# Optimization experiments

Hardware: AMD Instinct MI355X
Metric: run time of the kernel (lower is better)

Reference implementation:

```python
import jax, jax.numpy as jnp
import numpy as np

EPS = 1e-5
DIL = 1
PAD = 1
STRIDE = 1

def conv2d(x, w, stride=1, pad=1, dil=1):
    return jax.lax.conv_general_dilated(x, w, (stride, stride), [(pad, pad), (pad, pad)],
                                        rhs_dilation=(dil, dil),
                                        dimension_numbers=('NCHW', 'OIHW', 'NCHW'))

def batchnorm(x, g, b, m, v):
    inv = g / jnp.sqrt(v + EPS)
    return x * inv[None, :, None, None] + (b - m * inv)[None, :, None, None]

def _bilinear(img, y, x):
    # img: [C,H,W]; y,x: [Ho,Wo] float sample coords; zero padding outside.
    H, W = img.shape[1], img.shape[2]
    y0 = jnp.floor(y); x0 = jnp.floor(x)
    ty = y - y0; tx = x - x0
    y0i = y0.astype(jnp.int32); x0i = x0.astype(jnp.int32)
    def g(yi, xi):
        valid = (yi >= 0) & (yi < H) & (xi >= 0) & (xi < W)
        v = img[:, jnp.clip(yi, 0, H - 1), jnp.clip(xi, 0, W - 1)]  # [C,Ho,Wo]
        return jnp.where(valid[None], v, jnp.zeros((), img.dtype))
    return (g(y0i, x0i) * ((1 - ty) * (1 - tx))[None]
            + g(y0i, x0i + 1) * ((1 - ty) * tx)[None]
            + g(y0i + 1, x0i) * (ty * (1 - tx))[None]
            + g(y0i + 1, x0i + 1) * (ty * tx)[None])

def deform_conv(x, w, offset, stride=1, pad=1, dil=1):
    # offset: [B, 18, Ho, Wo], channels 0:9 = dy per kernel tap (row-major), 9:18 = dx.
    B, C, H, W = x.shape
    Co = w.shape[0]
    Ho = (H + 2 * pad - dil * 2 - 1) // stride + 1
    Wo = (W + 2 * pad - dil * 2 - 1) // stride + 1
    off = offset.reshape(B, 2, 9, Ho, Wo)
    iy = (jnp.arange(Ho) * stride - pad).astype(x.dtype)
    ix = (jnp.arange(Wo) * stride - pad).astype(x.dtype)
    wk = w.reshape(Co, C, 9)
    out = jnp.zeros((B, Co, Ho, Wo), x.dtype)
    for k in range(9):  # fixed 3x3 kernel taps
        ky, kx = k // 3, k % 3
        ys = iy[:, None] + ky * dil + off[:, 0, k]  # [B,Ho,Wo]
        xs = ix[None, :] + kx * dil + off[:, 1, k]
        val = jax.vmap(_bilinear)(x, ys, xs)        # [B,C,Ho,Wo]
        out = out + jnp.einsum('bchw,oc->bohw', val, wk[:, :, k])
    return out

def offset_bias(dil, dtype):
    bw = jnp.array([[-1., 0., 1.]] * 3, dtype) * (dil - 1)
    bh = bw.T
    return jnp.concatenate([bh.reshape(-1), bw.reshape(-1)])  # [18]

def setup_inputs() -> dict:
    key = jax.random.key(0)
    ks = jax.random.split(key, 12)
    B, C, H, W = 8, 256, 56, 56
    inp = {
        'x': jax.random.normal(ks[0], (B, C, H, W), jnp.float32),
        'conv1_w': jax.random.normal(ks[1], (C, C, 3, 3), jnp.float32) * 0.02,
        'bn1_g': jax.random.normal(ks[2], (C,), jnp.float32) * 0.1 + 1.0,
        'bn1_b': jax.random.normal(ks[3], (C,), jnp.float32) * 0.1,
        'bn1_m': jax.random.normal(ks[4], (C,), jnp.float32) * 0.1,
        'bn1_v': jax.random.uniform(ks[5], (C,), jnp.float32) + 0.5,
        'off_w': jax.random.normal(ks[6], (18, C, 3, 3), jnp.float32) * 0.01,
        'off_b': jnp.zeros((18,), jnp.float32),
        'conv2_w': jax.random.normal(ks[7], (C, C, 3, 3), jnp.float32) * 0.02,
        'bn2_g': jax.random.normal(ks[8], (C,), jnp.float32) * 0.1 + 1.0,
        'bn2_b': jax.random.normal(ks[9], (C,), jnp.float32) * 0.1,
        'bn2_m': jax.random.normal(ks[10], (C,), jnp.float32) * 0.1,
        'bn2_v': jax.random.uniform(ks[11], (C,), jnp.float32) + 0.5,
    }
    return inp

def reference(x, conv1_w, bn1_g, bn1_b, bn1_m, bn1_v, off_w, off_b, conv2_w, bn2_g, bn2_b, bn2_m, bn2_v):
    residual = x
    out = conv2d(x, conv1_w, STRIDE, PAD, DIL)
    out = jax.nn.relu(batchnorm(out, bn1_g, bn1_b, bn1_m, bn1_v))
    offset = conv2d(out, off_w, STRIDE, PAD, DIL) + off_b[None, :, None, None]
    offset = offset + offset_bias(DIL, out.dtype)[None, :, None, None]
    out = deform_conv(out, conv2_w, offset, STRIDE, PAD, DIL)
    out = batchnorm(out, bn2_g, bn2_b, bn2_m, bn2_v)
    return jax.nn.relu(out + residual)
```

## Files before the change

kernel.cpp:

```cpp
#include <hip/hip_runtime.h>
#include <hip/hip_fp16.h>

#define NB 8
#define NH 56
#define NW 56
#define NHW 3136
#define NCHW 802816
#define NPIX 25088
#define NHP 58
#define EPSV 1e-5f
#define BUFS 20480
#define TOFN 451584

typedef float f32x4 __attribute__((ext_vector_type(4)));
typedef __bf16 bf16x8 __attribute__((ext_vector_type(8)));
typedef _Float16 f16x8 __attribute__((ext_vector_type(8)));

__device__ __forceinline__ unsigned short f2b(float f) {
  unsigned int u = __float_as_uint(f);
  u += 0x7FFFu + ((u >> 16) & 1u);
  return (unsigned short)(u >> 16);
}
__device__ __forceinline__ unsigned short f2h(float f) {
  return __half_as_ushort(__float2half(f));
}
__device__ __forceinline__ void soft_barrier() {
  __builtin_amdgcn_s_waitcnt(0xC07F);
  __builtin_amdgcn_s_barrier();
}
__device__ __forceinline__ void dma16(const unsigned short* g, unsigned short* l) {
  __builtin_amdgcn_global_load_lds(
      (const __attribute__((address_space(1))) unsigned int*)g,
      (__attribute__((address_space(3))) unsigned int*)l,
      16, 0, 0);
}
__device__ __forceinline__ unsigned int bil2(
    unsigned int c00, unsigned int c01, unsigned int c10, unsigned int c11,
    __half2 W00, __half2 W01, __half2 W10, __half2 W11) {
  __half2 v = __hmul2(W00, *(__half2*)&c00);
  v = __hfma2(W01, *(__half2*)&c01, v);
  v = __hfma2(W10, *(__half2*)&c10, v);
  v = __hfma2(W11, *(__half2*)&c11, v);
  return *(unsigned int*)&v;
}

__global__ __launch_bounds__(256) void prep_fused(
    const float* __restrict__ x,  unsigned short* __restrict__ xbp,
    unsigned short* __restrict__ t1b, float* __restrict__ tof,
    const float* __restrict__ w1, const float* __restrict__ w2,
    const float* __restrict__ ow,
    unsigned short* __restrict__ w1p, unsigned short* __restrict__ w2p,
    unsigned short* __restrict__ w3p)
{
  __shared__ float T[64][65];
  const int bid = blockIdx.x;
  const int tid = threadIdx.x;

  if (bid < 228) {
    int i = bid*256 + tid;
    int q = i & 31; int pid = i >> 5;
    int b = pid / 228, j = pid % 228;
    int y, xx;
    if (j < 58)       { y = 0;  xx = j; }
    else if (j < 116) { y = 57; xx = j - 58; }
    else { int jj = j - 116; y = 1 + (jj >> 1); xx = (jj & 1) * 57; }
    size_t addr = ((size_t)(b*NHP + y)*NHP + xx)*256 + q*8;
    uint4 z = make_uint4(0u,0u,0u,0u);
    *(uint4*)(xbp + addr) = z;
    *(uint4*)(t1b + addr) = z;
    int zi = i*8;
    if (zi < TOFN) {
      *(float4*)(tof + zi)     = make_float4(0.f,0.f,0.f,0.f);
      *(float4*)(tof + zi + 4) = make_float4(0.f,0.f,0.f,0.f);
    }
  } else if (bid < 1796) {
    const int j2   = bid - 228;
    const int pxt  = (j2 % 392) * 64;
    const int cg   = (j2 / 392) * 64;
    const int b    = pxt / NHW;
    const int rem0 = pxt % NHW;
    const int pl   = tid & 63;
    const int c0   = tid >> 6;
    const float* src = x + (size_t)b*NCHW + rem0;
    #pragma unroll
    for (int it = 0; it < 16; ++it) {
      int c = c0 + it*4;
      T[c][pl] = src[(size_t)(cg + c)*NHW + pl];
    }
    __syncthreads();
    const int pr = tid >> 5;
    const int cp = tid & 31;
    #pragma unroll
    for (int it = 0; it < 8; ++it) {
      int pxl = pr + it*8;
      int rem = rem0 + pxl;
      int ho = rem / NW, wo = rem % NW;
      unsigned int pk = ((unsigned int)f2b(T[cp*2+1][pxl]) << 16) | (unsigned int)f2b(T[cp*2][pxl]);
      *(unsigned int*)(xbp + ((size_t)(b*NHP + ho + 1)*NHP + (wo + 1))*256 + cg + cp*2) = pk;
    }
  } else {
    int i = (bid - 1796)*256 + tid;
    if (i < 589824) {
      int co = i / 2304, r = i % 2304, k = r >> 8, ci = r & 255;
      w1p[i] = f2b(w1[((size_t)co*256 + ci)*9 + k]);
    } else if (i < 1179648) {
      int j = i - 589824;
      int co = j / 2304, r = j % 2304, k = r >> 8, ci = r & 255;
      w2p[j] = f2h(w2[((size_t)co*256 + ci)*9 + k]);
    } else {
      int j = i - 1179648;
      int co = j / 2304, r = j % 2304, k = r >> 8, ci = r & 255;
      w3p[j] = (co < 18) ? f2h(ow[((size_t)co*256 + ci)*9 + k]) : (unsigned short)0;
    }
  }
}

__global__ __launch_bounds__(512, 4) void gemm_conv1(
    const unsigned short* __restrict__ xbp, const unsigned short* __restrict__ w1p,
    const float* __restrict__ gam, const float* __restrict__ bet,
    const float* __restrict__ mu,  const float* __restrict__ var,
    unsigned short* __restrict__ t1b)
{
  __shared__ unsigned short SMEM[2*BUFS];

  const int bx   = blockIdx.x;
  const int nbx  = (bx & 7)*49 + (bx >> 3);
  const int m0   = nbx * 64;
  const int t    = threadIdx.x;
  const int lane = t & 63;
  const int wv   = t >> 6;
  const int wvM  = wv & 1;
  const int wvN  = wv >> 1;
  const int quad = lane >> 4;
  const int l15  = lane & 15;

  const int srow = t >> 3;
  const int seg  = t & 7;
  const int swz8 = ((seg ^ (srow & 7))*8);
  const int px  = m0 + srow;
  const int b   = px / NHW, rem = px % NHW;
  const int ho  = rem / NW, wo = rem % NW;
  const unsigned int pbaseA = ((unsigned int)(b*NHP + ho)*NHP + wo)*256u + (unsigned int)swz8;
  const int rowB0 = wv*32 + (lane >> 3);
  const unsigned int bswz = (unsigned int)(((lane & 7) ^ (lane >> 3))*8);
  const int chA = wv*512;

  f32x4 acc[2][4];
  #pragma unroll
  for (int i = 0; i < 2; ++i)
    #pragma unroll
    for (int j = 0; j < 4; ++j) acc[i][j] = (f32x4)(0.f);

  {
    dma16(xbp + pbaseA, &SMEM[chA]);
    #pragma unroll
    for (int j = 0; j < 4; ++j)
      dma16(w1p + (size_t)(rowB0 + j*8)*2304 + bswz, &SMEM[4096 + (wv*4 + j)*512]);
    __syncthreads();
  }

  for (int r = 0; r < 36; ++r) {
    unsigned short* Ac = SMEM + (r & 1)*BUFS;
    unsigned short* Bc = Ac + 4096;
    unsigned short* An = SMEM + ((r + 1) & 1)*BUFS;
    unsigned short* Bn = An + 4096;
    if (r < 35) {
      const int rn = r + 1;
      const int kn = rn >> 2, cicn = rn & 3;
      const int kyn = kn/3, kxn = kn - kyn*3;
      const unsigned int koff = (unsigned int)((kyn*NHP + kxn)*256 + cicn*64);
      dma16(xbp + pbaseA + koff, &An[chA]);
      const unsigned int rb = (unsigned int)(rn*64);
      #pragma unroll
      for (int j = 0; j < 4; ++j)
        dma16(w1p + (size_t)(rowB0 + j*8)*2304 + rb + bswz, &Bn[(wv*4 + j)*512]);
    }
    #pragma unroll
    for (int kk = 0; kk < 2; ++kk) {
      const int s8 = (kk*4 + quad) ^ (l15 & 7);
      bf16x8 af[2], bfr[4];
      #pragma unroll
      for (int mt = 0; mt < 2; ++mt)
        af[mt] = *(const bf16x8*)(&Ac[(wvM*32 + mt*16 + l15)*64 + s8*8]);
      #pragma unroll
      for (int nt = 0; nt < 4; ++nt)
        bfr[nt] = *(const bf16x8*)(&Bc[(wvN*64 + nt*16 + l15)*64 + s8*8]);
      #pragma unroll
      for (int mt = 0; mt < 2; ++mt)
        #pragma unroll
        for (int nt = 0; nt < 4; ++nt)
          acc[mt][nt] = __builtin_amdgcn_mfma_f32_16x16x32_bf16(af[mt], bfr[nt], acc[mt][nt], 0, 0, 0);
    }
    __syncthreads();
  }

  unsigned short* Sw = SMEM + wv*2304;
  #pragma unroll
  for (int nt = 0; nt < 4; ++nt) {
    const int co = wvN*64 + nt*16 + l15;
    const float inv  = gam[co] * rsqrtf(var[co] + EPSV);
    const float beta = bet[co] - mu[co]*inv;
    #pragma unroll
    for (int mt = 0; mt < 2; ++mt) {
      #pragma unroll
      for (int rr = 0; rr < 4; ++rr) {
        const int pxl = mt*16 + quad*4 + rr;
        float val = acc[mt][nt][rr]*inv + beta;
        val = val > 0.f ? val : 0.f;
        Sw[pxl*72 + nt*16 + l15] = f2h(val);
      }
    }
  }
  #pragma unroll
  for (int i = 0; i < 4; ++i) {
    const int pxl = (lane >> 3) + 8*i;
    const int sc  = lane & 7;
    uint4 q = *(const uint4*)(&Sw[pxl*72 + sc*8]);
    const int pg = m0 + wvM*32 + pxl;
    const int bb = pg / NHW, rm = pg % NHW;
    const int hh = rm / NW, ww = rm % NW;
    *(uint4*)(t1b + ((size_t)(bb*NHP + hh + 1)*NHP + ww + 1)*256 + wvN*64 + sc*8) = q;
  }
}

__global__ __launch_bounds__(256, 8) void gemm_off(
    const unsigned short* __restrict__ t1b, const unsigned short* __restrict__ w3p,
    const float* __restrict__ ob, float* __restrict__ toff)
{
  __shared__ unsigned short Al[4096];
  __shared__ unsigned short Bl[2048];

  const int bx  = blockIdx.x;
  const int nbx = (bx & 7)*49 + (bx >> 3);
  const int m0  = nbx * 64;
  const int kc = blockIdx.y;
  const int t    = threadIdx.x;
  const int lane = t & 63;
  const int wv   = t >> 6;
  const int quad = lane >> 4;
  const int l15  = lane & 15;

  const int arow = t >> 2;
  const int as4  = t & 3;
  const int axor = arow & 7;
  const int pxa  = m0 + arow;
  const int ba   = pxa / NHW, rema = pxa % NHW;
  const unsigned int pbase = ((unsigned int)(ba*NHP + rema/NW)*NHP + rema%NW)*256u;

  const int brow = t >> 3;
  const int bs   = t & 7;

  f32x4 acc[2];
  #pragma unroll
  for (int nt = 0; nt < 2; ++nt) {
    float init = 0.f;
    if (kc == 0) { int co = nt*16 + l15; init = (co < 18) ? ob[co] : 0.f; }
    acc[nt] = (f32x4)(init);
  }

  uint4 pA0, pA1, pB;
  {
    const int r = kc*9, k = r >> 2, cic = r & 3;
    const int ky = k/3, kx = k - ky*3;
    const unsigned int base = pbase + (unsigned int)((ky*NHP + kx)*256 + cic*64);
    pA0 = *(const uint4*)(t1b + base + as4*8);
    pA1 = *(const uint4*)(t1b + base + (as4+4)*8);
    pB  = *(const uint4*)(w3p + (size_t)brow*2304 + r*64 + bs*8);
  }

  for (int rr = 0; rr < 9; ++rr) {
    const int r = kc*9 + rr;
    __syncthreads();
    *(uint4*)(&Al[arow*64 + ((as4     ^ axor)*8)]) = pA0;
    *(uint4*)(&Al[arow*64 + (((as4+4) ^ axor)*8)]) = pA1;
    *(uint4*)(&Bl[brow*64 + ((bs ^ (brow & 7))*8)]) = pB;
    {
      const int rn = (rr < 8) ? r + 1 : r;
      const int kn = rn >> 2, cicn = rn & 3;
      const int kyn = kn/3, kxn = kn - kyn*3;
      const unsigned int base = pbase + (unsigned int)((kyn*NHP + kxn)*256 + cicn*64);
      pA0 = *(const uint4*)(t1b + base + as4*8);
      pA1 = *(const uint4*)(t1b + base + (as4+4)*8);
      pB  = *(const uint4*)(w3p + (size_t)brow*2304 + rn*64 + bs*8);
    }
    soft_barrier();
    #pragma unroll
    for (int kk = 0; kk < 2; ++kk) {
      const int s8 = (kk*4 + quad) ^ (l15 & 7);
      f16x8 af = *(const f16x8*)(&Al[(wv*16 + l15)*64 + s8*8]);
      #pragma unroll
      for (int nt = 0; nt < 2; ++nt) {
        f16x8 bfr = *(const f16x8*)(&Bl[(nt*16 + l15)*64 + s8*8]);
        acc[nt] = __builtin_amdgcn_mfma_f32_16x16x32_f16(af, bfr, acc[nt], 0, 0, 0);
      }
    }
  }
  #pragma unroll
  for (int nt = 0; nt < 2; ++nt) {
    const int co = nt*16 + l15;
    if (co < 18) {
      #pragma unroll
      for (int rr2 = 0; rr2 < 4; ++rr2) {
        const int pg = m0 + wv*16 + quad*4 + rr2;
        const int bb = pg / NHW, rm = pg % NHW;
        atomicAdd(&toff[(size_t)bb*(18*NHW) + (size_t)co*NHW + rm], acc[nt][rr2]);
      }
    }
  }
}

__global__ __launch_bounds__(512, 4) void gemm_deform(
    const unsigned short* __restrict__ t1b, const unsigned short* __restrict__ w2p,
    const float* __restrict__ toff, const float* __restrict__ xres,
    const float* __restrict__ gam, const float* __restrict__ bet,
    const float* __restrict__ mu,  const float* __restrict__ var,
    float* __restrict__ outp)
{
  __shared__ unsigned short SMEM[2*BUFS];

  const int bid  = blockIdx.x;
  const int nb   = (bid & 7)*49 + (bid >> 3);
  const int m0   = nb * 64;
  const int t    = threadIdx.x;
  const int lane = t & 63;
  const int wv   = t >> 6;
  const int wvM  = wv & 1;
  const int wvN  = wv >> 1;
  const int quad = lane >> 4;
  const int l15  = lane & 15;

  const int srow = t >> 3;
  const int seg  = t & 7;
  const int sxor = srow & 7;
  const int px   = m0 + srow;
  const int b    = px / NHW, rem = px % NHW;
  const int ho   = rem / NW, wo = rem % NW;
  const int obb  = b*(18*NHW) + rem;
  const unsigned int prowb = (unsigned int)(b*NHP);

  const int rowB0 = wv*32 + (lane >> 3);
  const unsigned int bswz = (unsigned int)(((lane & 7) ^ (lane >> 3))*8);

  f32x4 acc[2][4];
  #pragma unroll
  for (int i = 0; i < 2; ++i)
    #pragma unroll
    for (int j = 0; j < 4; ++j) acc[i][j] = (f32x4)(0.f);

  unsigned int o00, o01, o10, o11;
  __half2 W00, W01, W10, W11;
#define COORDS(KK) {                                                   \
    const int ky_ = (KK)/3, kx_ = (KK) - ky_*3;                        \
    const float offy = toff[obb + (KK)*NHW];                           \
    const float offx = toff[obb + (9+(KK))*NHW];                       \
    const float yf = (float)(ho - 1 + ky_) + offy;                     \
    const float xf = (float)(wo - 1 + kx_) + offx;                     \
    const float y0f = floorf(yf), x0f = floorf(xf);                    \
    const float ty = yf - y0f,   tx = xf - x0f;                        \
    const int y0p = (int)y0f + 1, x0p = (int)x0f + 1;                  \
    const int cy0 = min(max(y0p,   0), NHP-1);                         \
    const int cy1 = min(max(y0p+1, 0), NHP-1);                         \
    const int cx0 = min(max(x0p,   0), NHP-1);                         \
    const int cx1 = min(max(x0p+1, 0), NHP-1);                         \
    W00 = __float2half2_rn((1.f-ty)*(1.f-tx));                         \
    W01 = __float2half2_rn((1.f-ty)*tx);                               \
    W10 = __float2half2_rn(ty*(1.f-tx));                               \
    W11 = __float2half2_rn(ty*tx);                                     \
    o00 = ((prowb + cy0)*NHP + cx0)*256u + seg*8u;                     \
    o01 = ((prowb + cy0)*NHP + cx1)*256u + seg*8u;                     \
    o10 = ((prowb + cy1)*NHP + cx0)*256u + seg*8u;                     \
    o11 = ((prowb + cy1)*NHP + cx1)*256u + seg*8u;                     \
  }

#define PACKW(DST) {                                                            \
    uint4 res;                                                                  \
    res.x = bil2(pc00.x, pc01.x, pc10.x, pc11.x, W00, W01, W10, W11);           \
    res.y = bil2(pc00.y, pc01.y, pc10.y, pc11.y, W00, W01, W10, W11);           \
    res.z = bil2(pc00.z, pc01.z, pc10.z, pc11.z, W00, W01, W10, W11);           \
    res.w = bil2(pc00.w, pc01.w, pc10.w, pc11.w, W00, W01, W10, W11);           \
    *(uint4*)(&(DST)[srow*64 + ((seg ^ sxor)*8)]) = res;                        \
  }

#define ISSUEC(RN) {                                                           \
    const unsigned int cio_ = (unsigned int)(((RN) & 3)*64);                   \
    pc00 = *(const uint4*)(t1b + o00 + cio_);                                  \
    pc01 = *(const uint4*)(t1b + o01 + cio_);                                  \
    pc10 = *(const uint4*)(t1b + o10 + cio_);                                  \
    pc11 = *(const uint4*)(t1b + o11 + cio_);                                  \
  }

  uint4 pc00, pc01, pc10, pc11;

  COORDS(0);
  {
    ISSUEC(0);
    #pragma unroll
    for (int j = 0; j < 4; ++j)
      dma16(w2p + (size_t)(rowB0 + j*8)*2304 + bswz, &SMEM[4096 + (wv*4 + j)*512]);
    PACKW(SMEM);
    ISSUEC(1);
    __syncthreads();
  }

  for (int r = 0; r < 36; ++r) {
    unsigned short* Ac = SMEM + (r & 1)*BUFS;
    unsigned short* Bc = Ac + 4096;
    unsigned short* An = SMEM + ((r + 1) & 1)*BUFS;
    unsigned short* Bn = An + 4096;
    if (r < 35) PACKW(An);
    if (r < 35) {
      const unsigned int rb = (unsigned int)((r + 1)*64);
      #pragma unroll
      for (int j = 0; j < 4; ++j)
        dma16(w2p + (size_t)(rowB0 + j*8)*2304 + rb + bswz, &Bn[(wv*4 + j)*512]);
    }
    if ((r & 3) == 2 && r < 34) COORDS((r + 2) >> 2);
    if (r < 34) {
      ISSUEC(r + 2);
    }
    #pragma unroll
    for (int kk = 0; kk < 2; ++kk) {
      const int s8 = (kk*4 + quad) ^ (l15 & 7);
      f16x8 af[2], bfr[4];
      #pragma unroll
      for (int mt = 0; mt < 2; ++mt)
        af[mt] = *(const f16x8*)(&Ac[(wvM*32 + mt*16 + l15)*64 + s8*8]);
      #pragma unroll
      for (int nt = 0; nt < 4; ++nt)
        bfr[nt] = *(const f16x8*)(&Bc[(wvN*64 + nt*16 + l15)*64 + s8*8]);
      #pragma unroll
      for (int mt = 0; mt < 2; ++mt)
        #pragma unroll
        for (int nt = 0; nt < 4; ++nt)
          acc[mt][nt] = __builtin_amdgcn_mfma_f32_16x16x32_f16(af[mt], bfr[nt], acc[mt][nt], 0, 0, 0);
    }
    __syncthreads();
  }
#undef ISSUEC
#undef PACKW
#undef COORDS

  float* Sl = (float*)SMEM + wv*1056;
  const int pxl_r = lane & 31;
  const int csel  = lane >> 5;
  const int pg    = m0 + wvM*32 + pxl_r;
  const int bo    = pg / NHW, remo = pg % NHW;
  const size_t obase = (size_t)bo*NCHW + remo;
  #pragma unroll
  for (int h = 0; h < 2; ++h) {
    #pragma unroll
    for (int nt2 = 0; nt2 < 2; ++nt2) {
      const int nt = h*2 + nt2;
      #pragma unroll
      for (int mt = 0; mt < 2; ++mt) {
        #pragma unroll
        for (int rr = 0; rr < 4; ++rr) {
          const int pxl = mt*16 + quad*4 + rr;
          Sl[pxl*33 + nt2*16 + l15] = acc[mt][nt][rr];
        }
      }
    }
    #pragma unroll
    for (int j = 0; j < 16; ++j) {
      const int col = csel*16 + j;
      const int co  = wvN*64 + h*32 + col;
      const float inv  = gam[co] * rsqrtf(var[co] + EPSV);
      const float beta = bet[co] - mu[co]*inv;
      const size_t off = obase + (size_t)co*NHW;
      float val = Sl[pxl_r*33 + col];
      float o = val*inv + beta + xres[off];
      outp[off] = o > 0.f ? o : 0.f;
    }
  }
}

extern "C" void kernel_launch(void* const* d_in, const int* in_sizes, int n_in,
                              void* d_out, int out_size, void* d_ws, size_t ws_size,
                              hipStream_t stream) {
  const float* x   = (const float*)d_in[0];
  const float* w1  = (const float*)d_in[1];
  const float* g1  = (const float*)d_in[2];
  const float* b1  = (const float*)d_in[3];
  const float* m1  = (const float*)d_in[4];
  const float* v1  = (const float*)d_in[5];
  const float* ow  = (const float*)d_in[6];
  const float* ob  = (const float*)d_in[7];
  const float* w2  = (const float*)d_in[8];
  const float* g2  = (const float*)d_in[9];
  const float* b2  = (const float*)d_in[10];
  const float* m2  = (const float*)d_in[11];
  const float* v2  = (const float*)d_in[12];
  float* out = (float*)d_out;

  const size_t PADSZ = (size_t)NB*NHP*NHP*256;
  unsigned short* xbp = (unsigned short*)d_ws;
  unsigned short* t1b = xbp + PADSZ;
  float*          tof = (float*)(t1b + PADSZ);
  unsigned short* w1p = (unsigned short*)(tof + (size_t)NB*18*NHW);
  unsigned short* w2p = w1p + (size_t)589824;
  unsigned short* w3p = w2p + (size_t)589824;

  prep_fused<<<6692, 256, 0, stream>>>(x, xbp, t1b, tof, w1, w2, ow, w1p, w2p, w3p);

  gemm_conv1<<<392, 512, 0, stream>>>(xbp, w1p, g1, b1, m1, v1, t1b);
  dim3 go(392, 4, 1);
  gemm_off<<<go, 256, 0, stream>>>(t1b, w3p, ob, tof);
  gemm_deform<<<392, 512, 0, stream>>>(t1b, w2p, tof, x, g2, b2, m2, v2, out);
}
```

Baseline: 223.6 us.

## Split conv1 GEMM across output-channel halves and raise MFMA wave priority

The conv1 implicit GEMM now launches a second grid dimension, so each block computes 128 output channels instead of 256. This doubles the block count from 392 to 784 on a GPU with many CUs, and shrinks the B tile, the accumulators and the LDS footprint. The cost is that each A (activation) tile is loaded twice, once per channel half. Separately, s_setprio brackets the MFMA loops in both conv1 and the deform GEMM so compute waves get issue priority over waves doing loads.

```diff
diff --git a/kernel.cpp b/kernel.cpp
--- a/kernel.cpp
+++ b/kernel.cpp
@@ -10,6 +10,7 @@
 #define NHP 58
 #define EPSV 1e-5f
 #define BUFS 20480
+#define CBUF 12288
 #define TOFN 451584
 
 typedef float f32x4 __attribute__((ext_vector_type(4)));
@@ -115,17 +116,18 @@
   }
 }
 
-__global__ __launch_bounds__(512, 4) void gemm_conv1(
+__global__ __launch_bounds__(512, 3) void gemm_conv1(
     const unsigned short* __restrict__ xbp, const unsigned short* __restrict__ w1p,
     const float* __restrict__ gam, const float* __restrict__ bet,
     const float* __restrict__ mu,  const float* __restrict__ var,
     unsigned short* __restrict__ t1b)
 {
-  __shared__ unsigned short SMEM[2*BUFS];
+  __shared__ unsigned short SMEM[2*CBUF];
 
   const int bx   = blockIdx.x;
   const int nbx  = (bx & 7)*49 + (bx >> 3);
   const int m0   = nbx * 64;
+  const int n0   = blockIdx.y * 128;
   const int t    = threadIdx.x;
   const int lane = t & 63;
   const int wv   = t >> 6;
@@ -141,28 +143,28 @@
   const int b   = px / NHW, rem = px % NHW;
   const int ho  = rem / NW, wo = rem % NW;
   const unsigned int pbaseA = ((unsigned int)(b*NHP + ho)*NHP + wo)*256u + (unsigned int)swz8;
-  const int rowB0 = wv*32 + (lane >> 3);
+  const int rowB0 = wv*16 + (lane >> 3);
   const unsigned int bswz = (unsigned int)(((lane & 7) ^ (lane >> 3))*8);
   const int chA = wv*512;
 
-  f32x4 acc[2][4];
+  f32x4 acc[2][2];
   #pragma unroll
   for (int i = 0; i < 2; ++i)
     #pragma unroll
-    for (int j = 0; j < 4; ++j) acc[i][j] = (f32x4)(0.f);
+    for (int j = 0; j < 2; ++j) acc[i][j] = (f32x4)(0.f);
 
   {
     dma16(xbp + pbaseA, &SMEM[chA]);
     #pragma unroll
-    for (int j = 0; j < 4; ++j)
-      dma16(w1p + (size_t)(rowB0 + j*8)*2304 + bswz, &SMEM[4096 + (wv*4 + j)*512]);
+    for (int j = 0; j < 2; ++j)
+      dma16(w1p + (size_t)(n0 + rowB0 + j*8)*2304 + bswz, &SMEM[4096 + (wv*2 + j)*512]);
     __syncthreads();
   }
 
   for (int r = 0; r < 36; ++r) {
-    unsigned short* Ac = SMEM + (r & 1)*BUFS;
+    unsigned short* Ac = SMEM + (r & 1)*CBUF;
     unsigned short* Bc = Ac + 4096;
-    unsigned short* An = SMEM + ((r + 1) & 1)*BUFS;
+    unsigned short* An = SMEM + ((r + 1) & 1)*CBUF;
     unsigned short* Bn = An + 4096;
     if (r < 35) {
       const int rn = r + 1;
@@ -172,32 +174,34 @@
       dma16(xbp + pbaseA + koff, &An[chA]);
       const unsigned int rb = (unsigned int)(rn*64);
       #pragma unroll
-      for (int j = 0; j < 4; ++j)
-        dma16(w1p + (size_t)(rowB0 + j*8)*2304 + rb + bswz, &Bn[(wv*4 + j)*512]);
-    }
+      for (int j = 0; j < 2; ++j)
+        dma16(w1p + (size_t)(n0 + rowB0 + j*8)*2304 + rb + bswz, &Bn[(wv*2 + j)*512]);
+    }
+    __builtin_amdgcn_s_setprio(1);
     #pragma unroll
     for (int kk = 0; kk < 2; ++kk) {
       const int s8 = (kk*4 + quad) ^ (l15 & 7);
-      bf16x8 af[2], bfr[4];
+      bf16x8 af[2], bfr[2];
       #pragma unroll
       for (int mt = 0; mt < 2; ++mt)
         af[mt] = *(const bf16x8*)(&Ac[(wvM*32 + mt*16 + l15)*64 + s8*8]);
       #pragma unroll
-      for (int nt = 0; nt < 4; ++nt)
-        bfr[nt] = *(const bf16x8*)(&Bc[(wvN*64 + nt*16 + l15)*64 + s8*8]);
+      for (int nt = 0; nt < 2; ++nt)
+        bfr[nt] = *(const bf16x8*)(&Bc[(wvN*32 + nt*16 + l15)*64 + s8*8]);
       #pragma unroll
       for (int mt = 0; mt < 2; ++mt)
         #pragma unroll
-        for (int nt = 0; nt < 4; ++nt)
+        for (int nt = 0; nt < 2; ++nt)
           acc[mt][nt] = __builtin_amdgcn_mfma_f32_16x16x32_bf16(af[mt], bfr[nt], acc[mt][nt], 0, 0, 0);
     }
+    __builtin_amdgcn_s_setprio(0);
     __syncthreads();
   }
 
-  unsigned short* Sw = SMEM + wv*2304;
-  #pragma unroll
-  for (int nt = 0; nt < 4; ++nt) {
-    const int co = wvN*64 + nt*16 + l15;
+  unsigned short* Sw = SMEM + wv*1280;
+  #pragma unroll
+  for (int nt = 0; nt < 2; ++nt) {
+    const int co = n0 + wvN*32 + nt*16 + l15;
     const float inv  = gam[co] * rsqrtf(var[co] + EPSV);
     const float beta = bet[co] - mu[co]*inv;
     #pragma unroll
@@ -207,19 +211,19 @@
         const int pxl = mt*16 + quad*4 + rr;
         float val = acc[mt][nt][rr]*inv + beta;
         val = val > 0.f ? val : 0.f;
-        Sw[pxl*72 + nt*16 + l15] = f2h(val);
+        Sw[pxl*40 + nt*16 + l15] = f2h(val);
       }
     }
   }
   #pragma unroll
-  for (int i = 0; i < 4; ++i) {
-    const int pxl = (lane >> 3) + 8*i;
-    const int sc  = lane & 7;
-    uint4 q = *(const uint4*)(&Sw[pxl*72 + sc*8]);
+  for (int j = 0; j < 2; ++j) {
+    const int pxl  = lane >> 1;
+    const int colb = (lane & 1)*8 + j*16;
+    uint4 q = *(const uint4*)(&Sw[pxl*40 + colb]);
     const int pg = m0 + wvM*32 + pxl;
     const int bb = pg / NHW, rm = pg % NHW;
     const int hh = rm / NW, ww = rm % NW;
-    *(uint4*)(t1b + ((size_t)(bb*NHP + hh + 1)*NHP + ww + 1)*256 + wvN*64 + sc*8) = q;
+    *(uint4*)(t1b + ((size_t)(bb*NHP + hh + 1)*NHP + ww + 1)*256 + n0 + wvN*32 + colb) = q;
   }
 }
 
@@ -418,6 +422,7 @@
     if (r < 34) {
       ISSUEC(r + 2);
     }
+    __builtin_amdgcn_s_setprio(1);
     #pragma unroll
     for (int kk = 0; kk < 2; ++kk) {
       const int s8 = (kk*4 + quad) ^ (l15 & 7);
@@ -434,6 +439,7 @@
         for (int nt = 0; nt < 4; ++nt)
           acc[mt][nt] = __builtin_amdgcn_mfma_f32_16x16x32_f16(af[mt], bfr[nt], acc[mt][nt], 0, 0, 0);
     }
+    __builtin_amdgcn_s_setprio(0);
     __syncthreads();
   }
 #undef ISSUEC
@@ -502,7 +508,8 @@
 
   prep_fused<<<6692, 256, 0, stream>>>(x, xbp, t1b, tof, w1, w2, ow, w1p, w2p, w3p);
 
-  gemm_conv1<<<392, 512, 0, stream>>>(xbp, w1p, g1, b1, m1, v1, t1b);
+  dim3 g1d(392, 2, 1);
+  gemm_conv1<<<g1d, 512, 0, stream>>>(xbp, w1p, g1, b1, m1, v1, t1b);
   dim3 go(392, 4, 1);
   gemm_off<<<go, 256, 0, stream>>>(t1b, w3p, ob, tof);
   gemm_deform<<<392, 512, 0, stream>>>(t1b, w2p, tof, x, g2, b2, m2, v2, out);
```

Measured after the change: 232.6 us. 4.0% more time.
